# Kernel tuning notes

Hardware: AMD Instinct MI355X
Metric: run time of the kernel (lower is better)

The kernel has to match this reference:

```python
import jax, jax.numpy as jnp
import numpy as np


def _binarize(w):
    # sign(w) with sign(0) mapped to +1, matching the torch forward
    return jnp.where(w >= 0, 1.0, -1.0).astype(w.dtype)


def setup_inputs() -> dict:
    key = jax.random.key(0)
    k1, k2, k3 = jax.random.split(key, 3)
    N, IN, OUT = 8192, 4096, 4096
    x = jax.random.normal(k1, (N, IN), dtype=jnp.float32)
    weight = jax.random.normal(k2, (OUT, IN), dtype=jnp.float32)
    fan_in = IN
    bound = 1.0 / fan_in ** 0.5
    bias = jax.random.uniform(k3, (OUT,), dtype=jnp.float32, minval=-bound, maxval=bound)
    return {"x": x, "weight": weight, "bias": bias}


def reference(x, weight, bias):
    # forward: clamp(-1,1) then sign-binarize; clamp does not change the sign,
    # so binarized weight is simply sign(weight) with 0 -> +1.
    w_clamped = jnp.clip(weight, -1.0, 1.0)
    bw = _binarize(w_clamped)  # [OUT, IN] of +/-1
    # F.linear: x @ W^T + b
    return jnp.einsum('ni,oi->no', x, bw) + bias
```

## Files before the change

### kernel.cpp

```cpp
#include <hip/hip_runtime.h>
#include <stdint.h>

#define M_DIM 8192
#define N_DIM 4096
#define K_DIM 4096

typedef __attribute__((ext_vector_type(4))) int int32x4;

#define QUANT_BLOCKS 2048
#define SIGN_BLOCKS  1024
#define SIGN_THREADS (SIGN_BLOCKS * 256)

__global__ __launch_bounds__(256) void prep_kernel(const float* __restrict__ x,
                                                   const float* __restrict__ w,
                                                   signed char* __restrict__ xq,
                                                   signed char* __restrict__ wq,
                                                   float* __restrict__ scales) {
  const int bid = blockIdx.x;
  const int t = threadIdx.x;
  if (bid < QUANT_BLOCKS) {
    const int wave = t >> 6, lane = t & 63;
    const int row = bid * 4 + wave;
    const float4* xr = (const float4*)(x + (size_t)row * K_DIM);
    float4 v[16];
    float amax = 0.f;
#pragma unroll
    for (int j = 0; j < 16; j++) {
      v[j] = xr[lane + 64 * j];
      amax = fmaxf(amax, fmaxf(fmaxf(fabsf(v[j].x), fabsf(v[j].y)),
                               fmaxf(fabsf(v[j].z), fabsf(v[j].w))));
    }
#pragma unroll
    for (int off = 32; off > 0; off >>= 1)
      amax = fmaxf(amax, __shfl_xor(amax, off, 64));
    amax = fmaxf(amax, 1e-30f);
    const float rsc = 127.0f / amax;
    if (lane == 0) scales[row] = amax / 127.0f;
    int* qr = (int*)(xq + (size_t)row * K_DIM);
#pragma unroll
    for (int j = 0; j < 16; j++) {
      int q0 = __float2int_rn(v[j].x * rsc);
      int q1 = __float2int_rn(v[j].y * rsc);
      int q2 = __float2int_rn(v[j].z * rsc);
      int q3 = __float2int_rn(v[j].w * rsc);
      qr[lane + 64 * j] = (q0 & 255) | ((q1 & 255) << 8) | ((q2 & 255) << 16) | (q3 << 24);
    }
  } else {
    const int idx0 = (bid - QUANT_BLOCKS) * 256 + t;
    const float4* wf = (const float4*)w;
    int4* o = (int4*)wq;
#pragma unroll
    for (int k = 0; k < 4; k++) {
      const int idx = idx0 + k * SIGN_THREADS;
      int4 pk;
      int* pi = (int*)&pk;
#pragma unroll
      for (int j = 0; j < 4; j++) {
        float4 a = wf[(size_t)idx * 4 + j];
        unsigned b0 = a.x >= 0.f ? 0x01u : 0xFFu;
        unsigned b1 = a.y >= 0.f ? 0x01u : 0xFFu;
        unsigned b2 = a.z >= 0.f ? 0x01u : 0xFFu;
        unsigned b3 = a.w >= 0.f ? 0x01u : 0xFFu;
        pi[j] = (int)(b0 | (b1 << 8) | (b2 << 16) | (b3 << 24));
      }
      o[idx] = pk;
    }
  }
}

__device__ __forceinline__ void async16(const signed char* g, signed char* l) {
  __builtin_amdgcn_global_load_lds((const __attribute__((address_space(1))) void*)g,
                                   (__attribute__((address_space(3))) void*)l, 16, 0, 0);
}

__global__ __launch_bounds__(256) void gemm_i8_kernel(
    const signed char* __restrict__ A,
    const signed char* __restrict__ B,
    const float* __restrict__ scales,
    const float* __restrict__ bias,
    float* __restrict__ C) {
  __shared__ signed char la[128 * 64];
  __shared__ signed char lb[128 * 64];

  const int tid  = threadIdx.x;
  const int wave = tid >> 6;
  const int lane = tid & 63;
  const int wm = wave >> 1, wn = wave & 1;
  const int qd = lane >> 4, l16 = lane & 15;
  const long m0 = (long)blockIdx.y * 128;
  const long n0 = (long)blockIdx.x * 128;

  const int ch0 = wave * 128 + lane;
  const int ch1 = ch0 + 64;
  const signed char* ga0 = A + (m0 + (ch0 >> 2)) * K_DIM + (ch0 & 3) * 16;
  const signed char* ga1 = A + (m0 + (ch1 >> 2)) * K_DIM + (ch1 & 3) * 16;
  const signed char* gb0 = B + (n0 + (ch0 >> 2)) * K_DIM + (ch0 & 3) * 16;
  const signed char* gb1 = B + (n0 + (ch1 >> 2)) * K_DIM + (ch1 & 3) * 16;
  signed char* la0 = &la[(wave * 128) * 16];
  signed char* la1 = &la[(wave * 128 + 64) * 16];
  signed char* lb0 = &lb[(wave * 128) * 16];
  signed char* lb1 = &lb[(wave * 128 + 64) * 16];

  const int32x4* pa[4];
  const int32x4* pb[4];
#pragma unroll
  for (int t = 0; t < 4; t++) {
    pa[t] = (const int32x4*)&la[(wm * 64 + t * 16 + l16) * 64 + qd * 16];
    pb[t] = (const int32x4*)&lb[(wn * 64 + t * 16 + l16) * 64 + qd * 16];
  }

  int32x4 acc[4][4];
#pragma unroll
  for (int i = 0; i < 4; i++)
#pragma unroll
    for (int j = 0; j < 4; j++)
      acc[i][j] = (int32x4){0, 0, 0, 0};

  for (int k0 = 0; k0 < K_DIM; k0 += 64) {
    async16(ga0 + k0, la0);
    async16(ga1 + k0, la1);
    async16(gb0 + k0, lb0);
    async16(gb1 + k0, lb1);
    __syncthreads();

    int32x4 af[4], bf[4];
#pragma unroll
    for (int t = 0; t < 4; t++) { af[t] = *pa[t]; bf[t] = *pb[t]; }
#pragma unroll
    for (int i = 0; i < 4; i++)
#pragma unroll
      for (int j = 0; j < 4; j++)
        acc[i][j] = __builtin_amdgcn_mfma_i32_16x16x64_i8(af[i], bf[j], acc[i][j], 0, 0, 0);

    __syncthreads();
  }

  const long row0 = m0 + wm * 64 + qd * 4;
  const long col0 = n0 + wn * 64 + l16;
#pragma unroll
  for (int tj = 0; tj < 4; tj++) {
    float bv = bias[col0 + tj * 16];
#pragma unroll
    for (int ti = 0; ti < 4; ti++) {
      long r = row0 + ti * 16;
      float4 sv = *(const float4*)&scales[r];
      const float* s = &sv.x;
#pragma unroll
      for (int i = 0; i < 4; i++) {
        C[(r + i) * N_DIM + col0 + tj * 16] = (float)acc[ti][tj][i] * s[i] + bv;
      }
    }
  }
}

extern "C" void kernel_launch(void* const* d_in, const int* in_sizes, int n_in,
                              void* d_out, int out_size, void* d_ws, size_t ws_size,
                              hipStream_t stream) {
  const float* x    = (const float*)d_in[0];
  const float* w    = (const float*)d_in[1];
  const float* bias = (const float*)d_in[2];
  float* out = (float*)d_out;

  signed char* xq = (signed char*)d_ws;
  signed char* wq = xq + (size_t)M_DIM * K_DIM;
  float* scales   = (float*)(wq + (size_t)N_DIM * K_DIM);

  prep_kernel<<<QUANT_BLOCKS + SIGN_BLOCKS, 256, 0, stream>>>(x, w, xq, wq, scales);

  dim3 grid(N_DIM / 128, M_DIM / 128);
  gemm_i8_kernel<<<grid, 256, 0, stream>>>(xq, wq, scales, bias, out);
}
```

Before: 442.0 us.

## Double K-tile depth to 128 and XOR-swizzle LDS layout for int8 GEMM

Raises the per-iteration K tile from 64 to 128 bytes, so each block loads 32 KB of LDS per step and issues two MFMA sweeps between barriers. This halves the number of barrier pairs and async-load rounds. It also XOR-swizzles the 16-byte chunk position by row on both the global-to-LDS copy and the fragment reads, meant to remove LDS bank conflicts from the 128-byte row stride. In exchange it doubles shared memory per block, which may lower occupancy, and the load is still not double-buffered, so load latency stays exposed.

```diff
diff --git a/kernel.cpp b/kernel.cpp
--- a/kernel.cpp
+++ b/kernel.cpp
@@ -79,8 +79,8 @@
     const float* __restrict__ scales,
     const float* __restrict__ bias,
     float* __restrict__ C) {
-  __shared__ signed char la[128 * 64];
-  __shared__ signed char lb[128 * 64];
+  __shared__ signed char la[128 * 128];
+  __shared__ signed char lb[128 * 128];
 
   const int tid  = threadIdx.x;
   const int wave = tid >> 6;
@@ -90,23 +90,31 @@
   const long m0 = (long)blockIdx.y * 128;
   const long n0 = (long)blockIdx.x * 128;
 
-  const int ch0 = wave * 128 + lane;
-  const int ch1 = ch0 + 64;
-  const signed char* ga0 = A + (m0 + (ch0 >> 2)) * K_DIM + (ch0 & 3) * 16;
-  const signed char* ga1 = A + (m0 + (ch1 >> 2)) * K_DIM + (ch1 & 3) * 16;
-  const signed char* gb0 = B + (n0 + (ch0 >> 2)) * K_DIM + (ch0 & 3) * 16;
-  const signed char* gb1 = B + (n0 + (ch1 >> 2)) * K_DIM + (ch1 & 3) * 16;
-  signed char* la0 = &la[(wave * 128) * 16];
-  signed char* la1 = &la[(wave * 128 + 64) * 16];
-  signed char* lb0 = &lb[(wave * 128) * 16];
-  signed char* lb1 = &lb[(wave * 128 + 64) * 16];
+  const signed char* gA[4];
+  const signed char* gB[4];
+  signed char* lA[4];
+  signed char* lB[4];
+#pragma unroll
+  for (int q = 0; q < 4; q++) {
+    const int c = q * 256 + wave * 64 + lane;
+    const int r = c >> 3, s = c & 7;
+    const int off = (s ^ (r & 7)) * 16;
+    gA[q] = A + (m0 + r) * K_DIM + off;
+    gB[q] = B + (n0 + r) * K_DIM + off;
+    lA[q] = &la[(q * 256 + wave * 64) * 16];
+    lB[q] = &lb[(q * 256 + wave * 64) * 16];
+  }
 
-  const int32x4* pa[4];
-  const int32x4* pb[4];
+  const int swz = l16 & 7;
+  const int32x4* pa[4][2];
+  const int32x4* pb[4][2];
 #pragma unroll
   for (int t = 0; t < 4; t++) {
-    pa[t] = (const int32x4*)&la[(wm * 64 + t * 16 + l16) * 64 + qd * 16];
-    pb[t] = (const int32x4*)&lb[(wn * 64 + t * 16 + l16) * 64 + qd * 16];
+#pragma unroll
+    for (int kk = 0; kk < 2; kk++) {
+      pa[t][kk] = (const int32x4*)&la[(wm * 64 + t * 16 + l16) * 128 + ((kk * 4 + qd) ^ swz) * 16];
+      pb[t][kk] = (const int32x4*)&lb[(wn * 64 + t * 16 + l16) * 128 + ((kk * 4 + qd) ^ swz) * 16];
+    }
   }
 
   int32x4 acc[4][4];
@@ -116,21 +124,25 @@
     for (int j = 0; j < 4; j++)
       acc[i][j] = (int32x4){0, 0, 0, 0};
 
-  for (int k0 = 0; k0 < K_DIM; k0 += 64) {
-    async16(ga0 + k0, la0);
-    async16(ga1 + k0, la1);
-    async16(gb0 + k0, lb0);
-    async16(gb1 + k0, lb1);
+  for (int k0 = 0; k0 < K_DIM; k0 += 128) {
+#pragma unroll
+    for (int q = 0; q < 4; q++) {
+      async16(gA[q] + k0, lA[q]);
+      async16(gB[q] + k0, lB[q]);
+    }
     __syncthreads();
 
-    int32x4 af[4], bf[4];
 #pragma unroll
-    for (int t = 0; t < 4; t++) { af[t] = *pa[t]; bf[t] = *pb[t]; }
+    for (int kk = 0; kk < 2; kk++) {
+      int32x4 af[4], bf[4];
 #pragma unroll
-    for (int i = 0; i < 4; i++)
+      for (int t = 0; t < 4; t++) { af[t] = *pa[t][kk]; bf[t] = *pb[t][kk]; }
 #pragma unroll
-      for (int j = 0; j < 4; j++)
-        acc[i][j] = __builtin_amdgcn_mfma_i32_16x16x64_i8(af[i], bf[j], acc[i][j], 0, 0, 0);
+      for (int i = 0; i < 4; i++)
+#pragma unroll
+        for (int j = 0; j < 4; j++)
+          acc[i][j] = __builtin_amdgcn_mfma_i32_16x16x64_i8(af[i], bf[j], acc[i][j], 0, 0, 0);
+    }
 
     __syncthreads();
   }
```

New measurement: 403.3 us. 8.8% less time.
